# Optimization experiments

Hardware: AMD Instinct MI355X
Metric: run time of the kernel (lower is better)

## Reference

```python
import jax, jax.numpy as jnp
import numpy as np

N = 100000
E = 1600000
D = 128


def setup_inputs() -> dict:
    key = jax.random.key(0)
    ks = jax.random.split(key, 9)
    s = 1.0 / np.sqrt(D)
    return {
        "x": jax.random.normal(ks[0], (N, D), dtype=jnp.float32),
        "edge_index": jax.random.randint(ks[1], (2, E), 0, N, dtype=jnp.int64),
        # SAGEConv layer 1: lin_l (neighbor path, with bias), lin_r (root path, no bias)
        "Wl1": jax.random.normal(ks[2], (D, D), dtype=jnp.float32) * s,
        "bl1": jnp.zeros((D,), dtype=jnp.float32),
        "Wr1": jax.random.normal(ks[3], (D, D), dtype=jnp.float32) * s,
        # SAGEConv layer 2
        "Wl2": jax.random.normal(ks[4], (D, D), dtype=jnp.float32) * s,
        "bl2": jnp.zeros((D,), dtype=jnp.float32),
        "Wr2": jax.random.normal(ks[5], (D, D), dtype=jnp.float32) * s,
    }


def _sage_conv(x, src, dst, Wl, bl, Wr):
    # PyG SAGEConv, aggr='mean', root_weight=True:
    #   out = lin_l(mean_{j in N(i)} x_j) + lin_r(x_i)
    msg = x[src]                                              # [E, D] gather
    agg = jax.ops.segment_sum(msg, dst, num_segments=N)       # [N, D]
    cnt = jax.ops.segment_sum(jnp.ones((src.shape[0],), x.dtype), dst, num_segments=N)
    agg = agg / jnp.maximum(cnt, 1.0)[:, None]                # mean aggregation
    return agg @ Wl.T + bl + x @ Wr.T


def reference(x, edge_index, Wl1, bl1, Wr1, Wl2, bl2, Wr2):
    src, dst = edge_index[0], edge_index[1]
    h = jax.nn.relu(_sage_conv(x, src, dst, Wl1, bl1, Wr1))
    out = _sage_conv(h, src, dst, Wl2, bl2, Wr2)
    return out
```

## Files before the change

### kernel.cpp

```cpp
#include <hip/hip_runtime.h>
#include <stdint.h>

#define DN 128
#define NBITS 6
#define BNODES 64
#define HBMAX 2048
#define CAP 1536
#define NSL 256

__host__ __device__ static inline int divup(int a, int b){ return (a+b-1)/b; }

typedef __attribute__((ext_vector_type(8))) short bf16x8;
typedef __attribute__((ext_vector_type(4))) float floatx4;

__device__ __forceinline__ unsigned short f2bf(float f){
  unsigned int x = __float_as_uint(f);
  unsigned int r = x + 0x7fffu + ((x >> 16) & 1u);
  return (unsigned short)(r >> 16);
}
__device__ __forceinline__ unsigned int pack2(unsigned short a, unsigned short b){
  return (unsigned int)a | ((unsigned int)b << 16);
}

__global__ __launch_bounds__(256)
void convert_scatter(const float* __restrict__ x,
                     const float* __restrict__ w0, const float* __restrict__ w1,
                     const float* __restrict__ w2, const float* __restrict__ w3,
                     unsigned short* __restrict__ xb, unsigned short* __restrict__ Wb,
                     const int* __restrict__ src, const int* __restrict__ dst,
                     int* __restrict__ gcur, unsigned int* __restrict__ packed,
                     int E, int nbuck, int count8){
  __shared__ int h[HBMAX];
  __shared__ int cur[HBMAX];
  int t = threadIdx.x;

  if (blockIdx.x < NSL){
    int s = blockIdx.x;
    for (int i=t; i<nbuck; i+=256) h[i] = 0;
    __syncthreads();
    int n4 = E >> 2, per4 = divup(n4, NSL);
    int lo = s*per4, hi = min(lo+per4, n4);
    const int4* dst4 = (const int4*)dst;
    for (int i = lo + t; i < hi; i += 256){
      int4 d4 = dst4[i];
      atomicAdd(&h[d4.x >> NBITS], 1);
      atomicAdd(&h[d4.y >> NBITS], 1);
      atomicAdd(&h[d4.z >> NBITS], 1);
      atomicAdd(&h[d4.w >> NBITS], 1);
    }
    if (s == NSL-1){
      for (int e = (n4<<2) + t; e < E; e += 256)
        atomicAdd(&h[dst[e] >> NBITS], 1);
    }
    __syncthreads();
    for (int i=t; i<nbuck; i+=256){
      int c = h[i];
      int base = c ? atomicAdd(&gcur[i], c) : 0;
      cur[i] = i*CAP + base;
    }
    __syncthreads();
    const int4* src4 = (const int4*)src;
    for (int i = lo + t; i < hi; i += 256){
      int4 d4 = dst4[i];
      int4 s4 = src4[i];
      int dd[4] = {d4.x, d4.y, d4.z, d4.w};
      int ss[4] = {s4.x, s4.y, s4.z, s4.w};
      #pragma unroll
      for (int j=0;j<4;j++){
        int d = dd[j], b = d >> NBITS;
        int pos = atomicAdd(&cur[b], 1);
        if (pos < (b+1)*CAP)
          packed[pos] = (unsigned)ss[j] | ((unsigned)(d & (BNODES-1)) << 17);
      }
    }
    if (s == NSL-1){
      for (int e = (n4<<2) + t; e < E; e += 256){
        int d = dst[e], b = d >> NBITS;
        int pos = atomicAdd(&cur[b], 1);
        if (pos < (b+1)*CAP)
          packed[pos] = (unsigned)src[e] | ((unsigned)(d & (BNODES-1)) << 17);
      }
    }
  } else {
    int i = (blockIdx.x - NSL)*256 + t;
    const float* sp; unsigned short* dp; int off;
    if (i < count8){ sp = x; dp = xb; off = i; }
    else {
      int tid = i - count8;
      if (tid >= 8192) return;
      int mat = tid >> 11; off = tid & 2047;
      sp = (mat==0)?w0:(mat==1)?w1:(mat==2)?w2:w3;
      dp = Wb + (size_t)mat*16384;
    }
    const float4* sv = (const float4*)sp + (size_t)off*2;
    float4 a = sv[0], b = sv[1];
    uint4 o;
    o.x = pack2(f2bf(a.x), f2bf(a.y));
    o.y = pack2(f2bf(a.z), f2bf(a.w));
    o.z = pack2(f2bf(b.x), f2bf(b.y));
    o.w = pack2(f2bf(b.z), f2bf(b.w));
    ((uint4*)dp)[off] = o;
  }
}


__device__ __forceinline__
void node_sort_body(const int* __restrict__ gcur, unsigned int* __restrict__ buf,
                    int2* __restrict__ nodeOff2, int n){
  __shared__ int cnts[BNODES], cursor[BNODES];
  int b = blockIdx.x, t = threadIdx.x;
  int cnt = min(gcur[b], CAP);
  int base = b*CAP;
  if (t < BNODES) cnts[t] = 0;
  __syncthreads();
  unsigned pk[6];
  #pragma unroll
  for (int k=0;k<6;k++){
    int i = t + k*256;
    if (i < cnt){
      pk[k] = buf[base + i];
      atomicAdd(&cnts[(pk[k]>>17)&63], 1);
    }
  }
  __syncthreads();
  if (t < BNODES){
    int v = cnts[t], sft = v;
    #pragma unroll
    for (int off=1; off<64; off<<=1){
      int u = __shfl_up(sft, off, 64);
      if (t >= off) sft += u;
    }
    cursor[t] = sft - v;
    int node = b*BNODES + t;
    if (node < n) nodeOff2[node] = make_int2(base + sft - v, base + sft);
  }
  __syncthreads();
  #pragma unroll
  for (int k=0;k<6;k++){
    int i = t + k*256;
    if (i < cnt){
      int nd = (pk[k]>>17)&63;
      int r = atomicAdd(&cursor[nd], 1);
      buf[base + r] = pk[k] & 0x1FFFFu;
    }
  }
}

__device__ __forceinline__
void gemm_pre_body(int blk, const unsigned short* __restrict__ A,
                   const unsigned short* __restrict__ Wlb, const unsigned short* __restrict__ Wrb,
                   const float* __restrict__ bias,
                   unsigned short* __restrict__ y, unsigned short* __restrict__ z,
                   int rt_total, int rt_per_block)
{
  int t = threadIdx.x;
  int wave = t >> 6, lane = t & 63;
  int m = lane & 15, quad = lane >> 4;

  bf16x8 Bf[2][2][4];
  {
    const unsigned short* Ws[2] = {Wlb, Wrb};
    #pragma unroll
    for (int c2=0;c2<2;c2++){
      int col = wave*32 + c2*16 + m;
      #pragma unroll
      for (int mat=0;mat<2;mat++){
        const unsigned short* wrow = Ws[mat] + (size_t)col*DN + quad*8;
        #pragma unroll
        for (int kc=0;kc<4;kc++)
          Bf[c2][mat][kc] = *(const bf16x8*)(wrow + kc*32);
      }
    }
  }
  float bv0 = bias[wave*32 + m];
  float bv1 = bias[wave*32 + 16 + m];

  int rt_begin = blk * rt_per_block;
  int rt_end = rt_begin + rt_per_block; if (rt_end > rt_total) rt_end = rt_total;

  for (int rt = rt_begin; rt < rt_end; ++rt){
    const unsigned short* ap = A + ((size_t)(rt*16 + m))*DN + quad*8;
    bf16x8 Af[4];
    #pragma unroll
    for (int kc=0;kc<4;kc++) Af[kc] = *(const bf16x8*)(ap + kc*32);
    __syncthreads();
    floatx4 aY0 = {0.f,0.f,0.f,0.f}, aY1 = {0.f,0.f,0.f,0.f};
    floatx4 aZ0 = {0.f,0.f,0.f,0.f}, aZ1 = {0.f,0.f,0.f,0.f};
    #pragma unroll
    for (int kc=0; kc<4; kc++){
      aY0 = __builtin_amdgcn_mfma_f32_16x16x32_bf16(Af[kc], Bf[0][0][kc], aY0, 0,0,0);
      aY1 = __builtin_amdgcn_mfma_f32_16x16x32_bf16(Af[kc], Bf[1][0][kc], aY1, 0,0,0);
      aZ0 = __builtin_amdgcn_mfma_f32_16x16x32_bf16(Af[kc], Bf[0][1][kc], aZ0, 0,0,0);
      aZ1 = __builtin_amdgcn_mfma_f32_16x16x32_bf16(Af[kc], Bf[1][1][kc], aZ1, 0,0,0);
    }
    #pragma unroll
    for (int r=0;r<4;r++){
      int row = rt*16 + quad*4 + r;
      unsigned short* yo = y + (size_t)row*DN + wave*32 + m;
      yo[0]  = f2bf(aY0[r]);
      yo[16] = f2bf(aY1[r]);
      unsigned short* zo = z + (size_t)row*DN + wave*32 + m;
      zo[0]  = f2bf(aZ0[r] + bv0);
      zo[16] = f2bf(aZ1[r] + bv1);
    }
  }
}

__global__ __launch_bounds__(256)
void sort_gemm1(const int* __restrict__ gcur, unsigned int* __restrict__ buf,
                int2* __restrict__ nodeOff2, int n, int nbuck,
                const unsigned short* __restrict__ A,
                const unsigned short* __restrict__ Wlb, const unsigned short* __restrict__ Wrb,
                const float* __restrict__ bias,
                unsigned short* __restrict__ y, unsigned short* __restrict__ z,
                int rt_total, int rt_per_block)
{
  if ((int)blockIdx.x < nbuck)
    node_sort_body(gcur, buf, nodeOff2, n);
  else
    gemm_pre_body(blockIdx.x - nbuck, A, Wlb, Wrb, bias, y, z, rt_total, rt_per_block);
}

__global__ __launch_bounds__(256)
void gemm_pre(const unsigned short* __restrict__ A,
              const unsigned short* __restrict__ Wlb, const unsigned short* __restrict__ Wrb,
              const float* __restrict__ bias,
              unsigned short* __restrict__ y, unsigned short* __restrict__ z,
              int rt_total, int rt_per_block)
{
  gemm_pre_body(blockIdx.x, A, Wlb, Wrb, bias, y, z, rt_total, rt_per_block);
}

template<bool RELU, bool OUT_BF16>
__global__ __launch_bounds__(256)
void aggregate_pre(const unsigned short* __restrict__ yb, const unsigned short* __restrict__ zb,
                   const int2* __restrict__ nodeOff2, const unsigned int* __restrict__ csr_src,
                   void* __restrict__ out, int n){
  int g = (blockIdx.x*256 + threadIdx.x) >> 4;
  int l = threadIdx.x & 15;
  if (g >= n) return;
  int2 be = nodeOff2[g];
  int beg = be.x, end = be.y;
  float acc[8] = {0,0,0,0,0,0,0,0};
  #define ACCUM(u) { unsigned int w;                                   \
      w=(u).x; acc[0]+=__uint_as_float(w<<16); acc[1]+=__uint_as_float(w&0xffff0000u); \
      w=(u).y; acc[2]+=__uint_as_float(w<<16); acc[3]+=__uint_as_float(w&0xffff0000u); \
      w=(u).z; acc[4]+=__uint_as_float(w<<16); acc[5]+=__uint_as_float(w&0xffff0000u); \
      w=(u).w; acc[6]+=__uint_as_float(w<<16); acc[7]+=__uint_as_float(w&0xffff0000u); }
  int p = beg;
  for (; p+4 <= end; p += 4){
    int s0 = csr_src[p], s1 = csr_src[p+1], s2 = csr_src[p+2], s3 = csr_src[p+3];
    uint4 u0 = ((const uint4*)(yb + (size_t)s0*DN))[l];
    uint4 u1 = ((const uint4*)(yb + (size_t)s1*DN))[l];
    uint4 u2 = ((const uint4*)(yb + (size_t)s2*DN))[l];
    uint4 u3 = ((const uint4*)(yb + (size_t)s3*DN))[l];
    ACCUM(u0) ACCUM(u1) ACCUM(u2) ACCUM(u3)
  }
  for (; p < end; ++p){
    int s0 = csr_src[p];
    uint4 u0 = ((const uint4*)(yb + (size_t)s0*DN))[l];
    ACCUM(u0)
  }
  #undef ACCUM
  float inv = 1.f / fmaxf((float)(end-beg), 1.f);
  uint4 zc = ((const uint4*)(zb + (size_t)g*DN))[l];
  float v[8];
  { unsigned int w;
    w=zc.x; v[0]=__uint_as_float(w<<16); v[1]=__uint_as_float(w&0xffff0000u);
    w=zc.y; v[2]=__uint_as_float(w<<16); v[3]=__uint_as_float(w&0xffff0000u);
    w=zc.z; v[4]=__uint_as_float(w<<16); v[5]=__uint_as_float(w&0xffff0000u);
    w=zc.w; v[6]=__uint_as_float(w<<16); v[7]=__uint_as_float(w&0xffff0000u); }
  #pragma unroll
  for (int k=0;k<8;k++){
    v[k] += acc[k]*inv;
    if (RELU) v[k] = fmaxf(v[k], 0.f);
  }
  if (OUT_BF16){
    uint4 o;
    o.x = pack2(f2bf(v[0]), f2bf(v[1]));
    o.y = pack2(f2bf(v[2]), f2bf(v[3]));
    o.z = pack2(f2bf(v[4]), f2bf(v[5]));
    o.w = pack2(f2bf(v[6]), f2bf(v[7]));
    ((uint4*)((unsigned short*)out + (size_t)g*DN))[l] = o;
  } else {
    float* orow = (float*)out + (size_t)g*DN + l*8;
    float4 s0 = {v[0], v[1], v[2], v[3]};
    float4 s1 = {v[4], v[5], v[6], v[7]};
    ((float4*)orow)[0] = s0;
    ((float4*)orow)[1] = s1;
  }
}


extern "C" void kernel_launch(void* const* d_in, const int* in_sizes, int n_in,
                              void* d_out, int out_size, void* d_ws, size_t ws_size,
                              hipStream_t stream) {
  const float* x   = (const float*)d_in[0];
  const int*   ei  = (const int*)d_in[1];
  const float* Wl1 = (const float*)d_in[2];
  const float* bl1 = (const float*)d_in[3];
  const float* Wr1 = (const float*)d_in[4];
  const float* Wl2 = (const float*)d_in[5];
  const float* bl2 = (const float*)d_in[6];
  const float* Wr2 = (const float*)d_in[7];

  const int n = in_sizes[0] / DN;
  const int E = in_sizes[1] / 2;
  const int* src = ei;
  const int* dst = ei + E;
  const int nbuck = divup(n, BNODES);

  char* ws = (char*)d_ws;
  int* gcur = (int*)ws;  ws += (size_t)HBMAX*4;
  ws = (char*)(((uintptr_t)ws + 255) & ~(uintptr_t)255);
  unsigned int* packed = (unsigned int*)ws; ws += (size_t)nbuck*CAP*4;
  ws = (char*)(((uintptr_t)ws + 255) & ~(uintptr_t)255);
  int2* nodeOff2   = (int2*)ws; ws += (size_t)n*8;
  ws = (char*)(((uintptr_t)ws + 255) & ~(uintptr_t)255);
  unsigned short* Wb = (unsigned short*)ws; ws += 4*16384*2;
  unsigned short* xb = (unsigned short*)ws; ws += (size_t)n*DN*2;
  unsigned short* yb = (unsigned short*)ws; ws += (size_t)n*DN*2;
  unsigned short* hb = (unsigned short*)ws; ws += (size_t)n*DN*2;

  unsigned short* Wl1b = Wb;
  unsigned short* Wr1b = Wb + 16384;
  unsigned short* Wl2b = Wb + 2*16384;
  unsigned short* Wr2b = Wb + 3*16384;

  const int count8 = n*DN/8;
  const int rt_total = n / 16;
  const int rt_per_block = 5;
  const int gblocks = divup(rt_total, rt_per_block);
  const int agrid = divup(n*16, 256);

  hipMemsetAsync(gcur, 0, (size_t)HBMAX*4, stream);
  const int cgrid = NSL + divup(count8 + 8192, 256);
  convert_scatter<<<cgrid,256,0,stream>>>(x, Wl1, Wr1, Wl2, Wr2, xb, Wb,
                                          src, dst, gcur, packed, E, nbuck, count8);
  sort_gemm1<<<nbuck + gblocks,256,0,stream>>>(gcur, packed, nodeOff2, n, nbuck,
                                               xb, Wl1b, Wr1b, bl1, yb, xb,
                                               rt_total, rt_per_block);
  aggregate_pre<true, true ><<<agrid,256,0,stream>>>(yb, xb, nodeOff2, packed, hb, n);
  gemm_pre<<<gblocks,256,0,stream>>>(hb, Wl2b, Wr2b, bl2, yb, xb, rt_total, rt_per_block);
  aggregate_pre<false,false><<<agrid,256,0,stream>>>(yb, xb, nodeOff2, packed, d_out, n);
}
```

Baseline: 324.7 us.

## Fuse fp32-to-bf16 conversion into layer-1 GEMM and co-schedule it with edge scatter

Removes the separate pass that converted x and the weights to bf16. The first GEMM now reads fp32 x and fp32 weights directly and converts them in registers, and it runs in the same launch as the edge bucket scatter. Node sort moves to its own launch after that. This saves writing and re-reading a bf16 copy of x, and it also drops the redundant __syncthreads in the GEMM loop. In exchange the GEMM reads twice as many bytes for A and redoes the weight conversion in every block.

```diff
diff --git a/kernel.cpp b/kernel.cpp
--- a/kernel.cpp
+++ b/kernel.cpp
@@ -21,134 +21,71 @@
 __device__ __forceinline__ unsigned int pack2(unsigned short a, unsigned short b){
   return (unsigned int)a | ((unsigned int)b << 16);
 }
-
-__global__ __launch_bounds__(256)
-void convert_scatter(const float* __restrict__ x,
-                     const float* __restrict__ w0, const float* __restrict__ w1,
-                     const float* __restrict__ w2, const float* __restrict__ w3,
-                     unsigned short* __restrict__ xb, unsigned short* __restrict__ Wb,
-                     const int* __restrict__ src, const int* __restrict__ dst,
-                     int* __restrict__ gcur, unsigned int* __restrict__ packed,
-                     int E, int nbuck, int count8){
+__device__ __forceinline__ bf16x8 pack_bf8(float4 a, float4 b){
+  union { bf16x8 v; unsigned short u[8]; } r;
+  r.u[0]=f2bf(a.x); r.u[1]=f2bf(a.y); r.u[2]=f2bf(a.z); r.u[3]=f2bf(a.w);
+  r.u[4]=f2bf(b.x); r.u[5]=f2bf(b.y); r.u[6]=f2bf(b.z); r.u[7]=f2bf(b.w);
+  return r.v;
+}
+
+__device__ __forceinline__
+void scatter_body(const int* __restrict__ src, const int* __restrict__ dst,
+                  int* __restrict__ gcur, unsigned int* __restrict__ packed,
+                  int E, int nbuck){
   __shared__ int h[HBMAX];
   __shared__ int cur[HBMAX];
-  int t = threadIdx.x;
-
-  if (blockIdx.x < NSL){
-    int s = blockIdx.x;
-    for (int i=t; i<nbuck; i+=256) h[i] = 0;
-    __syncthreads();
-    int n4 = E >> 2, per4 = divup(n4, NSL);
-    int lo = s*per4, hi = min(lo+per4, n4);
-    const int4* dst4 = (const int4*)dst;
-    for (int i = lo + t; i < hi; i += 256){
-      int4 d4 = dst4[i];
-      atomicAdd(&h[d4.x >> NBITS], 1);
-      atomicAdd(&h[d4.y >> NBITS], 1);
-      atomicAdd(&h[d4.z >> NBITS], 1);
-      atomicAdd(&h[d4.w >> NBITS], 1);
-    }
-    if (s == NSL-1){
-      for (int e = (n4<<2) + t; e < E; e += 256)
-        atomicAdd(&h[dst[e] >> NBITS], 1);
-    }
-    __syncthreads();
-    for (int i=t; i<nbuck; i+=256){
-      int c = h[i];
-      int base = c ? atomicAdd(&gcur[i], c) : 0;
-      cur[i] = i*CAP + base;
-    }
-    __syncthreads();
-    const int4* src4 = (const int4*)src;
-    for (int i = lo + t; i < hi; i += 256){
-      int4 d4 = dst4[i];
-      int4 s4 = src4[i];
-      int dd[4] = {d4.x, d4.y, d4.z, d4.w};
-      int ss[4] = {s4.x, s4.y, s4.z, s4.w};
-      #pragma unroll
-      for (int j=0;j<4;j++){
-        int d = dd[j], b = d >> NBITS;
-        int pos = atomicAdd(&cur[b], 1);
-        if (pos < (b+1)*CAP)
-          packed[pos] = (unsigned)ss[j] | ((unsigned)(d & (BNODES-1)) << 17);
-      }
-    }
-    if (s == NSL-1){
-      for (int e = (n4<<2) + t; e < E; e += 256){
-        int d = dst[e], b = d >> NBITS;
-        int pos = atomicAdd(&cur[b], 1);
-        if (pos < (b+1)*CAP)
-          packed[pos] = (unsigned)src[e] | ((unsigned)(d & (BNODES-1)) << 17);
-      }
-    }
-  } else {
-    int i = (blockIdx.x - NSL)*256 + t;
-    const float* sp; unsigned short* dp; int off;
-    if (i < count8){ sp = x; dp = xb; off = i; }
-    else {
-      int tid = i - count8;
-      if (tid >= 8192) return;
-      int mat = tid >> 11; off = tid & 2047;
-      sp = (mat==0)?w0:(mat==1)?w1:(mat==2)?w2:w3;
-      dp = Wb + (size_t)mat*16384;
-    }
-    const float4* sv = (const float4*)sp + (size_t)off*2;
-    float4 a = sv[0], b = sv[1];
-    uint4 o;
-    o.x = pack2(f2bf(a.x), f2bf(a.y));
-    o.y = pack2(f2bf(a.z), f2bf(a.w));
-    o.z = pack2(f2bf(b.x), f2bf(b.y));
-    o.w = pack2(f2bf(b.z), f2bf(b.w));
-    ((uint4*)dp)[off] = o;
-  }
-}
-
-
+  int s = blockIdx.x, t = threadIdx.x;
+  for (int i=t; i<nbuck; i+=256) h[i] = 0;
+  __syncthreads();
+  int n4 = E >> 2, per4 = divup(n4, NSL);
+  int lo = s*per4, hi = min(lo+per4, n4);
+  const int4* dst4 = (const int4*)dst;
+  for (int i = lo + t; i < hi; i += 256){
+    int4 d4 = dst4[i];
+    atomicAdd(&h[d4.x >> NBITS], 1);
+    atomicAdd(&h[d4.y >> NBITS], 1);
+    atomicAdd(&h[d4.z >> NBITS], 1);
+    atomicAdd(&h[d4.w >> NBITS], 1);
+  }
+  if (s == NSL-1){
+    for (int e = (n4<<2) + t; e < E; e += 256)
+      atomicAdd(&h[dst[e] >> NBITS], 1);
+  }
+  __syncthreads();
+  for (int i=t; i<nbuck; i+=256){
+    int c = h[i];
+    int base = c ? atomicAdd(&gcur[i], c) : 0;
+    cur[i] = i*CAP + base;
+  }
+  __syncthreads();
+  const int4* src4 = (const int4*)src;
+  for (int i = lo + t; i < hi; i += 256){
+    int4 d4 = dst4[i];
+    int4 s4 = src4[i];
+    int dd[4] = {d4.x, d4.y, d4.z, d4.w};
+    int ss[4] = {s4.x, s4.y, s4.z, s4.w};
+    #pragma unroll
+    for (int j=0;j<4;j++){
+      int d = dd[j], b = d >> NBITS;
+      int pos = atomicAdd(&cur[b], 1);
+      if (pos < (b+1)*CAP)
+        packed[pos] = (unsigned)ss[j] | ((unsigned)(d & (BNODES-1)) << 17);
+    }
+  }
+  if (s == NSL-1){
+    for (int e = (n4<<2) + t; e < E; e += 256){
+      int d = dst[e], b = d >> NBITS;
+      int pos = atomicAdd(&cur[b], 1);
+      if (pos < (b+1)*CAP)
+        packed[pos] = (unsigned)src[e] | ((unsigned)(d & (BNODES-1)) << 17);
+    }
+  }
+}
+
+template<bool A_FP32>
 __device__ __forceinline__
-void node_sort_body(const int* __restrict__ gcur, unsigned int* __restrict__ buf,
-                    int2* __restrict__ nodeOff2, int n){
-  __shared__ int cnts[BNODES], cursor[BNODES];
-  int b = blockIdx.x, t = threadIdx.x;
-  int cnt = min(gcur[b], CAP);
-  int base = b*CAP;
-  if (t < BNODES) cnts[t] = 0;
-  __syncthreads();
-  unsigned pk[6];
-  #pragma unroll
-  for (int k=0;k<6;k++){
-    int i = t + k*256;
-    if (i < cnt){
-      pk[k] = buf[base + i];
-      atomicAdd(&cnts[(pk[k]>>17)&63], 1);
-    }
-  }
-  __syncthreads();
-  if (t < BNODES){
-    int v = cnts[t], sft = v;
-    #pragma unroll
-    for (int off=1; off<64; off<<=1){
-      int u = __shfl_up(sft, off, 64);
-      if (t >= off) sft += u;
-    }
-    cursor[t] = sft - v;
-    int node = b*BNODES + t;
-    if (node < n) nodeOff2[node] = make_int2(base + sft - v, base + sft);
-  }
-  __syncthreads();
-  #pragma unroll
-  for (int k=0;k<6;k++){
-    int i = t + k*256;
-    if (i < cnt){
-      int nd = (pk[k]>>17)&63;
-      int r = atomicAdd(&cursor[nd], 1);
-      buf[base + r] = pk[k] & 0x1FFFFu;
-    }
-  }
-}
-
-__device__ __forceinline__
-void gemm_pre_body(int blk, const unsigned short* __restrict__ A,
-                   const unsigned short* __restrict__ Wlb, const unsigned short* __restrict__ Wrb,
+void gemm_pre_body(int blk, const void* __restrict__ Araw,
+                   const float* __restrict__ Wl, const float* __restrict__ Wr,
                    const float* __restrict__ bias,
                    unsigned short* __restrict__ y, unsigned short* __restrict__ z,
                    int rt_total, int rt_per_block)
@@ -159,16 +96,17 @@
 
   bf16x8 Bf[2][2][4];
   {
-    const unsigned short* Ws[2] = {Wlb, Wrb};
+    const float* Ws[2] = {Wl, Wr};
     #pragma unroll
     for (int c2=0;c2<2;c2++){
       int col = wave*32 + c2*16 + m;
       #pragma unroll
       for (int mat=0;mat<2;mat++){
-        const unsigned short* wrow = Ws[mat] + (size_t)col*DN + quad*8;
+        const float* wrow = Ws[mat] + (size_t)col*DN + quad*8;
         #pragma unroll
         for (int kc=0;kc<4;kc++)
-          Bf[c2][mat][kc] = *(const bf16x8*)(wrow + kc*32);
+          Bf[c2][mat][kc] = pack_bf8(*(const float4*)(wrow + kc*32),
+                                     *(const float4*)(wrow + kc*32 + 4));
       }
     }
   }
@@ -179,11 +117,17 @@
   int rt_end = rt_begin + rt_per_block; if (rt_end > rt_total) rt_end = rt_total;
 
   for (int rt = rt_begin; rt < rt_end; ++rt){
-    const unsigned short* ap = A + ((size_t)(rt*16 + m))*DN + quad*8;
     bf16x8 Af[4];
-    #pragma unroll
-    for (int kc=0;kc<4;kc++) Af[kc] = *(const bf16x8*)(ap + kc*32);
-    __syncthreads();
+    if (A_FP32){
+      const float* ap = (const float*)Araw + (size_t)(rt*16 + m)*DN + quad*8;
+      #pragma unroll
+      for (int kc=0;kc<4;kc++)
+        Af[kc] = pack_bf8(*(const float4*)(ap + kc*32), *(const float4*)(ap + kc*32 + 4));
+    } else {
+      const unsigned short* ap = (const unsigned short*)Araw + (size_t)(rt*16 + m)*DN + quad*8;
+      #pragma unroll
+      for (int kc=0;kc<4;kc++) Af[kc] = *(const bf16x8*)(ap + kc*32);
+    }
     floatx4 aY0 = {0.f,0.f,0.f,0.f}, aY1 = {0.f,0.f,0.f,0.f};
     floatx4 aZ0 = {0.f,0.f,0.f,0.f}, aZ1 = {0.f,0.f,0.f,0.f};
     #pragma unroll
@@ -207,28 +151,71 @@
 }
 
 __global__ __launch_bounds__(256)
-void sort_gemm1(const int* __restrict__ gcur, unsigned int* __restrict__ buf,
-                int2* __restrict__ nodeOff2, int n, int nbuck,
-                const unsigned short* __restrict__ A,
-                const unsigned short* __restrict__ Wlb, const unsigned short* __restrict__ Wrb,
-                const float* __restrict__ bias,
-                unsigned short* __restrict__ y, unsigned short* __restrict__ z,
-                int rt_total, int rt_per_block)
+void scatter_gemm1(const int* __restrict__ src, const int* __restrict__ dst,
+                   int* __restrict__ gcur, unsigned int* __restrict__ packed,
+                   int E, int nbuck,
+                   const float* __restrict__ x,
+                   const float* __restrict__ Wl, const float* __restrict__ Wr,
+                   const float* __restrict__ bias,
+                   unsigned short* __restrict__ y, unsigned short* __restrict__ z,
+                   int rt_total, int rt_per_block)
 {
-  if ((int)blockIdx.x < nbuck)
-    node_sort_body(gcur, buf, nodeOff2, n);
+  if (blockIdx.x < NSL)
+    scatter_body(src, dst, gcur, packed, E, nbuck);
   else
-    gemm_pre_body(blockIdx.x - nbuck, A, Wlb, Wrb, bias, y, z, rt_total, rt_per_block);
+    gemm_pre_body<true>(blockIdx.x - NSL, x, Wl, Wr, bias, y, z, rt_total, rt_per_block);
 }
 
 __global__ __launch_bounds__(256)
-void gemm_pre(const unsigned short* __restrict__ A,
-              const unsigned short* __restrict__ Wlb, const unsigned short* __restrict__ Wrb,
-              const float* __restrict__ bias,
-              unsigned short* __restrict__ y, unsigned short* __restrict__ z,
-              int rt_total, int rt_per_block)
+void gemm_pre2(const unsigned short* __restrict__ A,
+               const float* __restrict__ Wl, const float* __restrict__ Wr,
+               const float* __restrict__ bias,
+               unsigned short* __restrict__ y, unsigned short* __restrict__ z,
+               int rt_total, int rt_per_block)
 {
-  gemm_pre_body(blockIdx.x, A, Wlb, Wrb, bias, y, z, rt_total, rt_per_block);
+  gemm_pre_body<false>(blockIdx.x, A, Wl, Wr, bias, y, z, rt_total, rt_per_block);
+}
+
+__global__ __launch_bounds__(256)
+void node_sort(const int* __restrict__ gcur, unsigned int* __restrict__ buf,
+               int2* __restrict__ nodeOff2, int n){
+  __shared__ int cnts[BNODES], cursor[BNODES];
+  int b = blockIdx.x, t = threadIdx.x;
+  int cnt = min(gcur[b], CAP);
+  int base = b*CAP;
+  if (t < BNODES) cnts[t] = 0;
+  __syncthreads();
+  unsigned pk[6];
+  #pragma unroll
+  for (int k=0;k<6;k++){
+    int i = t + k*256;
+    if (i < cnt){
+      pk[k] = buf[base + i];
+      atomicAdd(&cnts[(pk[k]>>17)&63], 1);
+    }
+  }
+  __syncthreads();
+  if (t < BNODES){
+    int v = cnts[t], sft = v;
+    #pragma unroll
+    for (int off=1; off<64; off<<=1){
+      int u = __shfl_up(sft, off, 64);
+      if (t >= off) sft += u;
+    }
+    cursor[t] = sft - v;
+    int node = b*BNODES + t;
+    if (node < n) nodeOff2[node] = make_int2(base + sft - v, base + sft);
+  }
+  __syncthreads();
+  #pragma unroll
+  for (int k=0;k<6;k++){
+    int i = t + k*256;
+    if (i < cnt){
+      int nd = (pk[k]>>17)&63;
+      int r = atomicAdd(&cursor[nd], 1);
+      buf[base + r] = pk[k] & 0x1FFFFu;
+    }
+  }
 }
 
 template<bool RELU, bool OUT_BF16>
@@ -317,30 +304,21 @@
   ws = (char*)(((uintptr_t)ws + 255) & ~(uintptr_t)255);
   int2* nodeOff2   = (int2*)ws; ws += (size_t)n*8;
   ws = (char*)(((uintptr_t)ws + 255) & ~(uintptr_t)255);
-  unsigned short* Wb = (unsigned short*)ws; ws += 4*16384*2;
-  unsigned short* xb = (unsigned short*)ws; ws += (size_t)n*DN*2;
+  unsigned short* zb = (unsigned short*)ws; ws += (size_t)n*DN*2;
   unsigned short* yb = (unsigned short*)ws; ws += (size_t)n*DN*2;
   unsigned short* hb = (unsigned short*)ws; ws += (size_t)n*DN*2;
 
-  unsigned short* Wl1b = Wb;
-  unsigned short* Wr1b = Wb + 16384;
-  unsigned short* Wl2b = Wb + 2*16384;
-  unsigned short* Wr2b = Wb + 3*16384;
-
-  const int count8 = n*DN/8;
   const int rt_total = n / 16;
   const int rt_per_block = 5;
   const int gblocks = divup(rt_total, rt_per_block);
   const int agrid = divup(n*16, 256);
 
   hipMemsetAsync(gcur, 0, (size_t)HBMAX*4, stream);
-  const int cgrid = NSL + divup(count8 + 8192, 256);
-  convert_scatter<<<cgrid,256,0,stream>>>(x, Wl1, Wr1, Wl2, Wr2, xb, Wb,
-                                          src, dst, gcur, packed, E, nbuck, count8);
-  sort_gemm1<<<nbuck + gblocks,256,0,stream>>>(gcur, packed, nodeOff2, n, nbuck,
-                                               xb, Wl1b, Wr1b, bl1, yb, xb,
-                                               rt_total, rt_per_block);
-  aggregate_pre<true, true ><<<agrid,256,0,stream>>>(yb, xb, nodeOff2, packed, hb, n);
-  gemm_pre<<<gblocks,256,0,stream>>>(hb, Wl2b, Wr2b, bl2, yb, xb, rt_total, rt_per_block);
-  aggregate_pre<false,false><<<agrid,256,0,stream>>>(yb, xb, nodeOff2, packed, d_out, n);
-}
+  scatter_gemm1<<<NSL + gblocks,256,0,stream>>>(src, dst, gcur, packed, E, nbuck,
+                                                x, Wl1, Wr1, bl1, yb, zb,
+                                                rt_total, rt_per_block);
+  node_sort<<<nbuck,256,0,stream>>>(gcur, packed, nodeOff2, n);
+  aggregate_pre<true, true ><<<agrid,256,0,stream>>>(yb, zb, nodeOff2, packed, hb, n);
+  gemm_pre2<<<gblocks,256,0,stream>>>(hb, Wl2, Wr2, bl2, yb, zb, rt_total, rt_per_block);
+  aggregate_pre<false,false><<<agrid,256,0,stream>>>(yb, zb, nodeOff2, packed, d_out, n);
+}
```

Result: slower. 344.7 us (+6.2%).
